# Optimization experiments

Hardware: AMD Instinct MI355X
Metric: run time of the kernel (lower is better)

The kernel has to match this reference:

```python
import jax, jax.numpy as jnp
import numpy as np

B, N, C, D, UP, KNN, MULT, PH = 4, 2048, 256, 64, 4, 20, 4, 64
EPS = 1e-5


def conv1d(x, w, b):
    # x: (B, Cin, N), w: (Cout, Cin)
    return jnp.einsum('oc,bcn->bon', w, x) + b[None, :, None]


def conv2d(x, w, b):
    # x: (B, Cin, N, K), 1x1 conv
    return jnp.einsum('oc,bcnk->bonk', w, x) + b[None, :, None, None]


def bn2d(x, g, bt, rm, rv):
    # eval-mode BatchNorm2d with running stats
    inv = jax.lax.rsqrt(rv + EPS)
    return g[None, :, None, None] * (x - rm[None, :, None, None]) * inv[None, :, None, None] + bt[None, :, None, None]


def group(f, idx):
    # f: (B, C, N), idx: (B, N, K) -> (B, C, N, K)
    return jax.vmap(lambda fb, ib: fb[:, ib])(f, idx)


def setup_inputs() -> dict:
    k0 = jax.random.key(0)
    ks = iter(jax.random.split(k0, 48))
    nx = lambda: next(ks)
    rn = lambda shape, s=0.05: jax.random.normal(nx(), shape, dtype=jnp.float32) * s
    z = lambda n: jnp.zeros((n,), jnp.float32)
    o = lambda n: jnp.ones((n,), jnp.float32)
    inp = {
        'pos': jax.random.normal(nx(), (B, 3, N), dtype=jnp.float32),
        'key': jax.random.normal(nx(), (B, C, N), dtype=jnp.float32),
        'query': jax.random.normal(nx(), (B, C, N), dtype=jnp.float32),
        # MLP_Res (mlp_v): in_dim=2C, hidden=C, out=C
        'wv1': rn((C, 2 * C)), 'bv1': z(C),
        'wv2': rn((C, C)), 'bv2': z(C),
        'wvs': rn((C, 2 * C)), 'bvs': z(C),
        # key/query/value projections to dim D
        'wk': rn((D, C)), 'bk': z(D),
        'wq': rn((D, C)), 'bq': z(D),
        'wval': rn((D, C)), 'bval': z(D),
        # pos_mlp: Conv2d(3,PH) -> BN -> ReLU -> Conv2d(PH,D)
        'pw1': rn((PH, 3)), 'pb1': z(PH), 'pg': o(PH), 'pbt': z(PH), 'prm': z(PH), 'prv': o(PH),
        'pw2': rn((D, PH)), 'pb2': z(D),
        # attn_mlp: Conv2d(D, D*MULT) -> BN -> ReLU -> ConvTranspose2d(D*MULT, D, (UP,1), (UP,1))
        'aw1': rn((D * MULT, D)), 'ab1': z(D * MULT), 'ag': o(D * MULT), 'abt': z(D * MULT), 'arm': z(D * MULT), 'arv': o(D * MULT),
        'ctw': rn((D * MULT, D, UP)), 'ctb': z(D),
        # conv_end: Conv1d(D, C)
        'we': rn((C, D)), 'be': z(C),
    }
    return inp


def reference(pos, key, query, wv1, bv1, wv2, bv2, wvs, bvs, wk, bk, wq, bq, wval, bval,
              pw1, pb1, pg, pbt, prm, prv, pw2, pb2,
              aw1, ab1, ag, abt, arm, arv, ctw, ctb, we, be):
    # mlp_v (MLP_Res) on concat([key, query])
    x = jnp.concatenate([key, query], axis=1)  # (B, 2C, N)
    value = conv1d(jax.nn.relu(conv1d(x, wv1, bv1)), wv2, bv2) + conv1d(x, wvs, bvs)  # (B, C, N)
    identity = value

    k_f = conv1d(key, wk, bk)      # (B, D, N)
    q_f = conv1d(query, wq, bq)    # (B, D, N)
    v_f = conv1d(value, wval, bval)

    # KNN (include_self=True): smallest-KNN indices of pairwise sq distance
    p = jnp.transpose(pos, (0, 2, 1))  # (B, N, 3)
    sq = jnp.sum(p * p, axis=-1)
    dist = sq[:, :, None] + sq[:, None, :] - 2.0 * jnp.einsum('bnc,bmc->bnm', p, p)
    idx = jax.lax.top_k(-dist, KNN)[1]  # (B, N, KNN)

    k_g = group(k_f, idx)                              # (B, D, N, KNN)
    qk_rel = q_f[:, :, :, None] - k_g
    pos_rel = pos[:, :, :, None] - group(pos, idx)     # (B, 3, N, KNN)

    h = jax.nn.relu(bn2d(conv2d(pos_rel, pw1, pb1), pg, pbt, prm, prv))
    pos_emb = conv2d(h, pw2, pb2)                      # (B, D, N, KNN)

    a = jax.nn.relu(bn2d(conv2d(qk_rel + pos_emb, aw1, ab1), ag, abt, arm, arv))  # (B, D*MULT, N, KNN)
    # ConvTranspose2d with kernel=(UP,1), stride=(UP,1): non-overlapping, out[b,o,n*UP+r,k]
    ct = jnp.einsum('bcnk,cor->bornk', a, ctw)         # (B, D, UP, N, KNN)
    Bv = a.shape[0]
    ct = jnp.transpose(ct, (0, 1, 3, 2, 4)).reshape(Bv, D, N * UP, KNN) + ctb[None, :, None, None]
    attn = jax.nn.softmax(ct, axis=-1)                 # softmax over neighbors

    v_g = group(v_f, idx) + pos_emb                    # (B, D, N, KNN)
    v_up = jnp.repeat(v_g, UP, axis=2)                 # nearest Upsample (UP,1)
    agg = jnp.sum(attn * v_up, axis=-1)                # (B, D, N*UP)
    y = conv1d(agg, we, be)                            # (B, C, N*UP)
    return y + jnp.repeat(identity, UP, axis=2)
```

## Files before the change

kernel.cpp:

```cpp
#include <hip/hip_runtime.h>
#include <hip/hip_bf16.h>

#define Bq 4
#define Nq 2048
#define Cq 256
#define Dq 64
#define UPq 4
#define KNNq 20
#define PHq 64
#define DMq 256
#define PTS 16

typedef __attribute__((ext_vector_type(8))) short short8;
typedef __attribute__((ext_vector_type(4))) short short4v;
typedef __attribute__((ext_vector_type(4))) float f32x4;
typedef __hip_bfloat16 bf16;

__device__ __forceinline__ void ld16(float* d, const float* s){
  *reinterpret_cast<float4*>(d) = *reinterpret_cast<const float4*>(s);
}
__device__ __forceinline__ unsigned short f2b(float x){
  bf16 h = __float2bfloat16(x);
  return *reinterpret_cast<unsigned short*>(&h);
}
__device__ __forceinline__ float b2f(short s){
  return __bfloat162float(*reinterpret_cast<bf16*>(&s));
}

__device__ __forceinline__ void swz(const float* __restrict__ src,
                                    short* __restrict__ dst,
                                    int M, int K, int g, bool transp)
{
  int j = g & 7, lane = (g >> 3) & 63, rest = g >> 9;
  int KS = K >> 5;
  int ks = rest % KS, mt = rest / KS;
  int m = mt*16 + (lane & 15);
  int k = ks*32 + ((lane >> 4) << 3) + j;
  float v = transp ? src[k*M + m] : src[m*K + k];
  dst[g] = (short)f2b(v);
}

__global__ __launch_bounds__(256) void k_prep(
    const float* __restrict__ aw1, const float* __restrict__ ctw,
    const float* __restrict__ wv1, const float* __restrict__ wvs,
    const float* __restrict__ wv2, const float* __restrict__ wk,
    const float* __restrict__ wq,  const float* __restrict__ wval,
    const float* __restrict__ pw2, const float* __restrict__ we,
    short* __restrict__ aw1b, short* __restrict__ ctwT,
    short* __restrict__ wv1b, short* __restrict__ wvsb,
    short* __restrict__ wv2b, short* __restrict__ wkb,
    short* __restrict__ wqb,  short* __restrict__ wvalb,
    short* __restrict__ pw2b, short* __restrict__ web)
{
  const int t = threadIdx.x, bidx = blockIdx.x;
  if (bidx < 512){
    swz(wv1, wv1b, 256, 512, bidx*256 + t, false);
  } else if (bidx < 1024){
    swz(wvs, wvsb, 256, 512, (bidx-512)*256 + t, false);
  } else if (bidx < 1280){
    swz(wv2, wv2b, 256, 256, (bidx-1024)*256 + t, false);
  } else if (bidx < 1344){
    swz(wk, wkb, 64, 256, (bidx-1280)*256 + t, false);
  } else if (bidx < 1408){
    swz(wq, wqb, 64, 256, (bidx-1344)*256 + t, false);
  } else if (bidx < 1472){
    swz(wval, wvalb, 64, 256, (bidx-1408)*256 + t, false);
  } else if (bidx < 1488){
    swz(pw2, pw2b, 64, 64, (bidx-1472)*256 + t, false);
  } else if (bidx < 1552){
    swz(aw1, aw1b, 256, 64, (bidx-1488)*256 + t, false);
  } else if (bidx < 1616){
    swz(we, web, 256, 64, (bidx-1552)*256 + t, false);
  } else {
    swz(ctw, ctwT, 256, 256, (bidx-1616)*256 + t, true);
  }
}

__global__ __launch_bounds__(256) void k_value(
    const float* __restrict__ key, const float* __restrict__ query,
    const short* __restrict__ wv1b, const short* __restrict__ wvsb,
    const short* __restrict__ wv2b, const short* __restrict__ wkb,
    const short* __restrict__ wqb,  const short* __restrict__ wvalb,
    const float* __restrict__ bv1, const float* __restrict__ bv2,
    const float* __restrict__ bvs, const float* __restrict__ bk,
    const float* __restrict__ bq,  const float* __restrict__ bval,
    float* __restrict__ valueT, short* __restrict__ kfT,
    short* __restrict__ qfT,    short* __restrict__ vfT)
{
  __shared__ __align__(16) short Xb[16*520];
  __shared__ __align__(16) short hidB[16*264];
  __shared__ __align__(16) short valB[16*264];
  __shared__ __align__(16) float valF[16*264];
  const int t = threadIdx.x;
  const int b = blockIdx.x >> 7;
  const int n0 = (blockIdx.x & 127) * PTS;
  const int lane = t & 63, quad = lane >> 4, l15 = lane & 15, w = t >> 6;

  {
    const int c4 = t >> 2, pq = t & 3;
    #pragma unroll
    for (int pass=0; pass<4; pass++){
      int c = pass*64 + c4;
      float4 kv = *reinterpret_cast<const float4*>(key   + ((size_t)(b*Cq+c))*Nq + n0 + pq*4);
      float4 qv = *reinterpret_cast<const float4*>(query + ((size_t)(b*Cq+c))*Nq + n0 + pq*4);
      const float* kf_ = (const float*)&kv;
      const float* qf_ = (const float*)&qv;
      #pragma unroll
      for (int i=0;i<4;i++){
        Xb[(pq*4+i)*520 + c]       = (short)f2b(kf_[i]);
        Xb[(pq*4+i)*520 + 256 + c] = (short)f2b(qf_[i]);
      }
    }
  }
  __syncthreads();

  f32x4 acc1[4], accS[4];
  #pragma unroll
  for (int jm=0;jm<4;jm++){ acc1[jm]=(f32x4)0.f; accS[jm]=(f32x4)0.f; }

  #pragma unroll
  for (int ks=0;ks<16;ks++){
    const int kcol = ks*32 + quad*8;
    short8 xb = *reinterpret_cast<const short8*>(&Xb[l15*520 + kcol]);
    #pragma unroll
    for (int jm=0;jm<4;jm++){
      int mt = w*4 + jm;
      short8 a1 = *reinterpret_cast<const short8*>(wv1b + ((mt*16+ks)*64 + lane)*8);
      short8 as = *reinterpret_cast<const short8*>(wvsb + ((mt*16+ks)*64 + lane)*8);
      acc1[jm] = __builtin_amdgcn_mfma_f32_16x16x32_bf16(a1, xb, acc1[jm], 0,0,0);
      accS[jm] = __builtin_amdgcn_mfma_f32_16x16x32_bf16(as, xb, accS[jm], 0,0,0);
    }
  }
  #pragma unroll
  for (int jm=0;jm<4;jm++){
    #pragma unroll
    for (int r=0;r<4;r++){
      int h = (w*4+jm)*16 + quad*4 + r;
      hidB[l15*264 + h] = (short)f2b(fmaxf(acc1[jm][r] + bv1[h], 0.f));
    }
  }
  __syncthreads();

  #pragma unroll
  for (int ks=0;ks<8;ks++){
    const int kcol = ks*32 + quad*8;
    short8 hb = *reinterpret_cast<const short8*>(&hidB[l15*264 + kcol]);
    #pragma unroll
    for (int jm=0;jm<4;jm++){
      int mt = w*4 + jm;
      short8 a = *reinterpret_cast<const short8*>(wv2b + ((mt*8+ks)*64 + lane)*8);
      accS[jm] = __builtin_amdgcn_mfma_f32_16x16x32_bf16(a, hb, accS[jm], 0,0,0);
    }
  }
  #pragma unroll
  for (int jm=0;jm<4;jm++){
    #pragma unroll
    for (int r=0;r<4;r++){
      int c = (w*4+jm)*16 + quad*4 + r;
      float v = accS[jm][r] + bv2[c] + bvs[c];
      valF[l15*264 + c] = v;
      valB[l15*264 + c] = (short)f2b(v);
    }
  }
  __syncthreads();

  #pragma unroll
  for (int p=0;p<PTS;p++)
    valueT[((size_t)(b*Nq + n0 + p))*Cq + t] = valF[p*264 + t];

  {
    f32x4 pk4=(f32x4)0.f, pq4=(f32x4)0.f, pv4=(f32x4)0.f;
    #pragma unroll
    for (int ks=0;ks<8;ks++){
      const int kcol = ks*32 + quad*8;
      short8 xk = *reinterpret_cast<const short8*>(&Xb[l15*520 + kcol]);
      short8 xq = *reinterpret_cast<const short8*>(&Xb[l15*520 + 256 + kcol]);
      short8 xv = *reinterpret_cast<const short8*>(&valB[l15*264 + kcol]);
      short8 ak = *reinterpret_cast<const short8*>(wkb  + ((w*8+ks)*64 + lane)*8);
      short8 aq = *reinterpret_cast<const short8*>(wqb  + ((w*8+ks)*64 + lane)*8);
      short8 av = *reinterpret_cast<const short8*>(wvalb+ ((w*8+ks)*64 + lane)*8);
      pk4 = __builtin_amdgcn_mfma_f32_16x16x32_bf16(ak, xk, pk4, 0,0,0);
      pq4 = __builtin_amdgcn_mfma_f32_16x16x32_bf16(aq, xq, pq4, 0,0,0);
      pv4 = __builtin_amdgcn_mfma_f32_16x16x32_bf16(av, xv, pv4, 0,0,0);
    }
    short4v ok, oq, ov;
    #pragma unroll
    for (int r=0;r<4;r++){
      int o = w*16 + quad*4 + r;
      ok[r] = (short)f2b(pk4[r] + bk[o]);
      oq[r] = (short)f2b(pq4[r] + bq[o]);
      ov[r] = (short)f2b(pv4[r] + bval[o]);
    }
    int n = n0 + l15;
    size_t base = ((size_t)(b*Nq+n))*Dq + w*16 + quad*4;
    *reinterpret_cast<short4v*>(kfT + base) = ok;
    *reinterpret_cast<short4v*>(qfT + base) = oq;
    *reinterpret_cast<short4v*>(vfT + base) = ov;
  }
}

__global__ __launch_bounds__(256) void k_knn(const float* __restrict__ pos,
                                             int* __restrict__ idxT)
{
  const int t = threadIdx.x;
  const int lane = t & 63;
  const int w = t >> 6;
  const int pid = blockIdx.x*4 + w;
  const int b = pid >> 11;
  const int n = pid & (Nq-1);
  const float* px = pos + (size_t)(b*3+0)*Nq;
  const float* py = pos + (size_t)(b*3+1)*Nq;
  const float* pz = pos + (size_t)(b*3+2)*Nq;
  const float xn=px[n], yn=py[n], zn=pz[n];
  const float sqn = __fadd_rn(__fadd_rn(__fmul_rn(xn,xn),__fmul_rn(yn,yn)),__fmul_rn(zn,zn));

  double kd[32];
  #pragma unroll
  for (int i=0;i<32;i++){
    int j = i*64 + lane;
    float x=px[j], y=py[j], z=pz[j];
    float sqj = __fadd_rn(__fadd_rn(__fmul_rn(x,x),__fmul_rn(y,y)),__fmul_rn(z,z));
    float dot = __fadd_rn(__fadd_rn(__fmul_rn(xn,x),__fmul_rn(yn,y)),__fmul_rn(zn,z));
    float d   = __fsub_rn(__fadd_rn(sqn,sqj), __fmul_rn(2.0f,dot));
    unsigned u = __float_as_uint(d);
    u ^= ((unsigned)((int)u >> 31)) | 0x80000000u;
    kd[i] = (double)u * 2048.0 + (double)j;
  }

  const double BIG = 9.0e15;
  double last = -1.0;
  for (int s=0;s<KNNq;s++){
    double c[16];
    #pragma unroll
    for (int i=0;i<16;i++){
      double a0 = (kd[i]    > last) ? kd[i]    : BIG;
      double a1 = (kd[i+16] > last) ? kd[i+16] : BIG;
      c[i] = fmin(a0, a1);
    }
    #pragma unroll
    for (int off=8; off>0; off>>=1){
      #pragma unroll
      for (int i=0;i<off;i++) c[i] = fmin(c[i], c[i+off]);
    }
    double m = c[0];
    #pragma unroll
    for (int off=1; off<64; off<<=1)
      m = fmin(m, __shfl_xor(m, off));
    if (lane == 0){
      unsigned long long kk = (unsigned long long)m;
      idxT[(size_t)pid*KNNq + s] = (int)(kk & 2047ull);
    }
    last = m;
  }
}

__global__ __launch_bounds__(256) void k_attn(
  const float* __restrict__ pos,
  const float* __restrict__ valueT, const short* __restrict__ kfT,
  const short* __restrict__ qfT,    const short* __restrict__ vfT,
  const int* __restrict__ idxT,
  const float* __restrict__ pw1, const float* __restrict__ pb1,
  const float* __restrict__ pg,  const float* __restrict__ pbt,
  const float* __restrict__ prm, const float* __restrict__ prv,
  const short* __restrict__ pw2b, const float* __restrict__ pb2,
  const short* __restrict__ aw1b, const float* __restrict__ ab1,
  const float* __restrict__ ag,  const float* __restrict__ abt,
  const float* __restrict__ arm, const float* __restrict__ arv,
  const short* __restrict__ ctwT,
  const short* __restrict__ web,  const float* __restrict__ be,
  float* __restrict__ out)
{
  __shared__ __align__(16) char  unionA[26624];
  __shared__ __align__(16) char  unionB[6912];
  __shared__ __align__(16) short uT[48*72];
  __shared__ __align__(16) short vgB[64*56];
  __shared__ float scS[DMq], sh2S[DMq];
  __shared__ float prl[3*48];
  __shared__ int   nb[48];

  short* sT   = (short*)unionA;
  short* ctS  = (short*)unionA;
  short* hB   = (short*)unionB;
  short* aggB = (short*)unionB;

  const int t = threadIdx.x;
  const int b  = blockIdx.x >> 10;
  const int n0 = (blockIdx.x & 1023) * 2;
  const int lane = t & 63, quad = lane >> 4, l15 = lane & 15, w = t >> 6;
  const size_t bN = (size_t)b * Nq;

  if (t < 48){
    int p = (t >= 24);
    int k = t - p*24;
    int nn = n0 + p;
    int j = (k < KNNq) ? idxT[(bN + nn)*KNNq + k] : nn;
    nb[t] = j;
    #pragma unroll
    for (int d=0; d<3; d++){
      prl[d*48+t] = pos[((size_t)(b*3+d))*Nq + nn] - pos[((size_t)(b*3+d))*Nq + j];
    }
  }
  {
    float sc = ag[t] * rsqrtf(arv[t] + 1e-5f);
    scS[t]  = sc;
    sh2S[t] = ab1[t]*sc + (abt[t] - arm[t]*sc);
  }
  __syncthreads();

  {
    const int ph = t & 63, pkq = t >> 6;
    float sc = pg[ph] * rsqrtf(prv[ph] + 1e-5f);
    float sh = pbt[ph] - prm[ph] * sc;
    float w0 = pw1[ph*3+0], w1 = pw1[ph*3+1], w2 = pw1[ph*3+2];
    float bb = pb1[ph];
    #pragma unroll
    for (int m=0;m<12;m++){
      int pk = pkq + m*4;
      float h = w0*prl[pk] + w1*prl[48+pk] + w2*prl[96+pk] + bb;
      hB[pk*72 + ph] = (short)f2b(fmaxf(h*sc + sh, 0.f));
    }
  }
  __syncthreads();

  {
    f32x4 accP[3];
    #pragma unroll
    for (int nt=0;nt<3;nt++) accP[nt]=(f32x4)0.f;
    #pragma unroll
    for (int ks=0;ks<2;ks++){
      const int kcol = ks*32 + quad*8;
      short8 a = *reinterpret_cast<const short8*>(pw2b + ((w*2+ks)*64 + lane)*8);
      #pragma unroll
      for (int nt=0;nt<3;nt++){
        short8 bb = *reinterpret_cast<const short8*>(&hB[(nt*16+l15)*72 + kcol]);
        accP[nt] = __builtin_amdgcn_mfma_f32_16x16x32_bf16(a, bb, accP[nt], 0,0,0);
      }
    }
    const int obase = w*16 + quad*4;
    #pragma unroll
    for (int nt=0;nt<3;nt++){
      int pk = nt*16 + l15;
      int p = (pk >= 24);
      int j = nb[pk];
      int nn = n0 + p;
      short4v q4 = *reinterpret_cast<const short4v*>(qfT + (bN+nn)*Dq + obase);
      short4v k4 = *reinterpret_cast<const short4v*>(kfT + (bN+j)*Dq + obase);
      short4v v4 = *reinterpret_cast<const short4v*>(vfT + (bN+j)*Dq + obase);
      #pragma unroll
      for (int r=0;r<4;r++){
        int o = obase + r;
        float pe = accP[nt][r] + pb2[o];
        uT[pk*72 + o]  = (short)f2b((b2f(q4[r]) - b2f(k4[r])) + pe);
        vgB[o*56 + pk] = (short)f2b(b2f(v4[r]) + pe);
      }
    }
  }
  __syncthreads();

  {
    for (int i = t; i < 576; i += 256) aggB[576 + i] = 0;

    f32x4 accC[4][3];
    #pragma unroll
    for (int jm=0;jm<4;jm++)
      #pragma unroll
      for (int nt=0;nt<3;nt++) accC[jm][nt]=(f32x4)0.f;
    #pragma unroll
    for (int ks=0;ks<2;ks++){
      const int kcol = ks*32 + quad*8;
      short8 bb[3];
      #pragma unroll
      for (int nt=0;nt<3;nt++)
        bb[nt] = *reinterpret_cast<const short8*>(&uT[(nt*16+l15)*72 + kcol]);
      #pragma unroll
      for (int jm=0;jm<4;jm++){
        int mt = w*4 + jm;
        short8 a = *reinterpret_cast<const short8*>(aw1b + ((mt*2+ks)*64 + lane)*8);
        #pragma unroll
        for (int nt=0;nt<3;nt++)
          accC[jm][nt] = __builtin_amdgcn_mfma_f32_16x16x32_bf16(a, bb[nt], accC[jm][nt], 0,0,0);
      }
    }
    #pragma unroll
    for (int jm=0;jm<4;jm++){
      int cb = (w*4+jm)*16 + quad*4;
      #pragma unroll
      for (int nt=0;nt<3;nt++){
        int pk = nt*16 + l15;
        short4v pkv;
        #pragma unroll
        for (int r=0;r<4;r++){
          int c = cb + r;
          pkv[r] = (short)f2b(fmaxf(accC[jm][nt][r]*scS[c] + sh2S[c], 0.f));
        }
        *reinterpret_cast<short4v*>(&sT[pk*264 + cb]) = pkv;
      }
    }
  }
  __syncthreads();

  {
    f32x4 accT[4][3];
    #pragma unroll
    for (int jm=0;jm<4;jm++)
      #pragma unroll
      for (int nt=0;nt<3;nt++) accT[jm][nt]=(f32x4)0.f;
    #pragma unroll
    for (int ks=0;ks<8;ks++){
      const int kcol = ks*32 + quad*8;
      short8 bb[3];
      #pragma unroll
      for (int nt=0;nt<3;nt++)
        bb[nt] = *reinterpret_cast<const short8*>(&sT[(nt*16+l15)*264 + kcol]);
      #pragma unroll
      for (int jm=0;jm<4;jm++){
        int mt = w*4 + jm;
        short8 a = *reinterpret_cast<const short8*>(ctwT + ((mt*8+ks)*64 + lane)*8);
        #pragma unroll
        for (int nt=0;nt<3;nt++)
          accT[jm][nt] = __builtin_amdgcn_mfma_f32_16x16x32_bf16(a, bb[nt], accT[jm][nt], 0,0,0);
      }
    }
    __syncthreads();
    #pragma unroll
    for (int jm=0;jm<4;jm++){
      #pragma unroll
      for (int nt=0;nt<3;nt++){
        int pk = nt*16 + l15;
        #pragma unroll
        for (int r=0;r<4;r++){
          int row = (w*4+jm)*16 + quad*4 + r;
          ctS[row*52 + pk] = (short)f2b(accT[jm][nt][r]);
        }
      }
    }
  }
  __syncthreads();

  {
    int o = t >> 2, rr = t & 3;
    #pragma unroll
    for (int p=0;p<2;p++){
      float ct[20], vgv[20];
      #pragma unroll
      for (int q=0;q<5;q++){
        short4v cv  = *reinterpret_cast<const short4v*>(&ctS[t*52 + p*24 + q*4]);
        short4v vv4 = *reinterpret_cast<const short4v*>(&vgB[o*56 + p*24 + q*4]);
        #pragma unroll
        for (int i=0;i<4;i++){ ct[q*4+i]=b2f(cv[i]); vgv[q*4+i]=b2f(vv4[i]); }
      }
      float m = ct[0];
      #pragma unroll
      for (int k=1;k<20;k++) m = fmaxf(m, ct[k]);
      float s = 0.f, a = 0.f;
      #pragma unroll
      for (int k=0;k<20;k++){
        float e = __expf(ct[k]-m);
        s += e;
        a = fmaf(e, vgv[k], a);
      }
      aggB[(p*4+rr)*72 + o] = (short)f2b(a/s);
    }
  }
  __syncthreads();

  {
    f32x4 accE[4];
    #pragma unroll
    for (int jm=0;jm<4;jm++) accE[jm]=(f32x4)0.f;
    #pragma unroll
    for (int ks=0;ks<2;ks++){
      const int kcol = ks*32 + quad*8;
      short8 bb = *reinterpret_cast<const short8*>(&aggB[l15*72 + kcol]);
      #pragma unroll
      for (int jm=0;jm<4;jm++){
        int mt = w*4 + jm;
        short8 a = *reinterpret_cast<const short8*>(web + ((mt*2+ks)*64 + lane)*8);
        accE[jm] = __builtin_amdgcn_mfma_f32_16x16x32_bf16(a, bb, accE[jm], 0,0,0);
      }
    }
    if (l15 < 8){
      int p = l15 >> 2, rr = l15 & 3;
      #pragma unroll
      for (int jm=0;jm<4;jm++){
        #pragma unroll
        for (int r=0;r<4;r++){
          int c = (w*4+jm)*16 + quad*4 + r;
          float y = accE[jm][r] + be[c] + valueT[(bN + n0 + p)*Cq + c];
          out[((size_t)(b*Cq+c))*((size_t)Nq*UPq) + (size_t)(n0+p)*UPq + rr] = y;
        }
      }
    }
  }
}

extern "C" void kernel_launch(void* const* d_in, const int* in_sizes, int n_in,
                              void* d_out, int out_size, void* d_ws, size_t ws_size,
                              hipStream_t stream)
{
  const float* pos  = (const float*)d_in[0];
  const float* key  = (const float*)d_in[1];
  const float* qry  = (const float*)d_in[2];
  const float* wv1  = (const float*)d_in[3];
  const float* bv1  = (const float*)d_in[4];
  const float* wv2  = (const float*)d_in[5];
  const float* bv2  = (const float*)d_in[6];
  const float* wvs  = (const float*)d_in[7];
  const float* bvs  = (const float*)d_in[8];
  const float* wk   = (const float*)d_in[9];
  const float* bk   = (const float*)d_in[10];
  const float* wq   = (const float*)d_in[11];
  const float* bq   = (const float*)d_in[12];
  const float* wval = (const float*)d_in[13];
  const float* bval = (const float*)d_in[14];
  const float* pw1  = (const float*)d_in[15];
  const float* pb1  = (const float*)d_in[16];
  const float* pg   = (const float*)d_in[17];
  const float* pbt  = (const float*)d_in[18];
  const float* prm  = (const float*)d_in[19];
  const float* prv  = (const float*)d_in[20];
  const float* pw2  = (const float*)d_in[21];
  const float* pb2  = (const float*)d_in[22];
  const float* aw1  = (const float*)d_in[23];
  const float* ab1  = (const float*)d_in[24];
  const float* ag   = (const float*)d_in[25];
  const float* abt  = (const float*)d_in[26];
  const float* arm  = (const float*)d_in[27];
  const float* arv  = (const float*)d_in[28];
  const float* ctw  = (const float*)d_in[29];
  const float* we   = (const float*)d_in[31];
  const float* be   = (const float*)d_in[32];

  char* ws = (char*)d_ws;
  float* valueT = (float*)(ws);
  short* kfT    = (short*)(ws + 8388608);
  short* qfT    = (short*)(ws + 9437184);
  short* vfT    = (short*)(ws + 10485760);
  int*   idxT   = (int*)  (ws + 11534336);
  short* aw1b   = (short*)(ws + 12189696);
  short* ctwT   = (short*)(ws + 12222464);
  short* wv1b   = (short*)(ws + 12353536);
  short* wvsb   = (short*)(ws + 12615680);
  short* wv2b   = (short*)(ws + 12877824);
  short* wkb    = (short*)(ws + 13008896);
  short* wqb    = (short*)(ws + 13041664);
  short* wvalb  = (short*)(ws + 13074432);
  short* pw2b   = (short*)(ws + 13107200);
  short* web    = (short*)(ws + 13115392);
  float* out    = (float*)d_out;

  k_prep<<<dim3(1872), dim3(256), 0, stream>>>(
      aw1, ctw, wv1, wvs, wv2, wk, wq, wval, pw2, we,
      aw1b, ctwT, wv1b, wvsb, wv2b, wkb, wqb, wvalb, pw2b, web);
  k_value<<<dim3(Bq*Nq/PTS), dim3(256), 0, stream>>>(
      key, qry, wv1b, wvsb, wv2b, wkb, wqb, wvalb,
      bv1, bv2, bvs, bk, bq, bval,
      valueT, kfT, qfT, vfT);
  k_knn<<<dim3(Bq*Nq/4), dim3(256), 0, stream>>>(pos, idxT);
  k_attn<<<dim3(Bq*Nq/2), dim3(256), 0, stream>>>(
      pos, valueT, kfT, qfT, vfT, idxT,
      pw1, pb1, pg, pbt, prm, prv, pw2b, pb2,
      aw1b, ab1, ag, abt, arm, arv, ctwT, web, be, out);
}
```

Measured before the change: 286.5 us.

## Shrink attention kernel LDS footprint via chunked MLP, swizzling, and BN folding

Restructures k_attn so the attn_mlp hidden activations are produced and consumed in two 128-channel chunks, which lets the shared-memory buffers shrink and be unioned, and sets launch bounds to target 4 blocks per CU. LDS layouts switch from padded strides to XOR-swizzled addressing. BatchNorm scale is folded into aw1 during prep and into pw1 inside the kernel. Neighbor gathers and identity loads are issued early to hide latency, and only the 20 valid neighbor columns are stored. The trade-off is an extra barrier per chunk and higher register pressure from the hoisted loads.

```diff
diff --git a/kernel.cpp b/kernel.cpp
--- a/kernel.cpp
+++ b/kernel.cpp
@@ -40,6 +40,21 @@
   dst[g] = (short)f2b(v);
 }
 
+__device__ __forceinline__ void swz_s(const float* __restrict__ src,
+                                      short* __restrict__ dst,
+                                      int M, int K, int g,
+                                      const float* __restrict__ gam,
+                                      const float* __restrict__ var)
+{
+  int j = g & 7, lane = (g >> 3) & 63, rest = g >> 9;
+  int KS = K >> 5;
+  int ks = rest % KS, mt = rest / KS;
+  int m = mt*16 + (lane & 15);
+  int k = ks*32 + ((lane >> 4) << 3) + j;
+  float sc = gam[m] * rsqrtf(var[m] + 1e-5f);
+  dst[g] = (short)f2b(src[m*K + k] * sc);
+}
+
 __global__ __launch_bounds__(256) void k_prep(
     const float* __restrict__ aw1, const float* __restrict__ ctw,
     const float* __restrict__ wv1, const float* __restrict__ wvs,
@@ -50,7 +65,8 @@
     short* __restrict__ wv1b, short* __restrict__ wvsb,
     short* __restrict__ wv2b, short* __restrict__ wkb,
     short* __restrict__ wqb,  short* __restrict__ wvalb,
-    short* __restrict__ pw2b, short* __restrict__ web)
+    short* __restrict__ pw2b, short* __restrict__ web,
+    const float* __restrict__ ag, const float* __restrict__ arv)
 {
   const int t = threadIdx.x, bidx = blockIdx.x;
   if (bidx < 512){
@@ -68,7 +84,7 @@
   } else if (bidx < 1488){
     swz(pw2, pw2b, 64, 64, (bidx-1472)*256 + t, false);
   } else if (bidx < 1552){
-    swz(aw1, aw1b, 256, 64, (bidx-1488)*256 + t, false);
+    swz_s(aw1, aw1b, 256, 64, (bidx-1488)*256 + t, ag, arv);
   } else if (bidx < 1616){
     swz(we, web, 256, 64, (bidx-1552)*256 + t, false);
   } else {
@@ -254,7 +270,10 @@
   }
 }
 
-__global__ __launch_bounds__(256) void k_attn(
+#define UADDR(row, colb) ((((row)*128 + (colb)) ^ (((row)&7)<<4)))
+#define SADDR(row, colb) ((((row)*256 + (colb)) ^ (((row)&7)<<4)))
+
+__global__ __launch_bounds__(256, 4) void k_attn(
   const float* __restrict__ pos,
   const float* __restrict__ valueT, const short* __restrict__ kfT,
   const short* __restrict__ qfT,    const short* __restrict__ vfT,
@@ -270,24 +289,21 @@
   const short* __restrict__ web,  const float* __restrict__ be,
   float* __restrict__ out)
 {
-  __shared__ __align__(16) char  unionA[26624];
-  __shared__ __align__(16) char  unionB[6912];
-  __shared__ __align__(16) short uT[48*72];
-  __shared__ __align__(16) short vgB[64*56];
-  __shared__ float scS[DMq], sh2S[DMq];
-  __shared__ float prl[3*48];
-  __shared__ int   nb[48];
-
-  short* sT   = (short*)unionA;
-  short* ctS  = (short*)unionA;
-  short* hB   = (short*)unionB;
-  short* aggB = (short*)unionB;
+  __shared__ __align__(16) char unionA[22528];
+  __shared__ __align__(16) char unionB[6144];
+  __shared__ __align__(16) char unionC[6144];
+  __shared__ __align__(16) short vgB[64*40];
+
+  float* sh2S = (float*)(unionA + 12288);
+  float* prl  = (float*)unionC;
+  int*   nb   = (int*)(unionC + 576);
 
   const int t = threadIdx.x;
   const int b  = blockIdx.x >> 10;
   const int n0 = (blockIdx.x & 1023) * 2;
   const int lane = t & 63, quad = lane >> 4, l15 = lane & 15, w = t >> 6;
   const size_t bN = (size_t)b * Nq;
+  const int obase = w*16 + quad*4;
 
   if (t < 48){
     int p = (t >= 24);
@@ -302,22 +318,31 @@
   }
   {
     float sc = ag[t] * rsqrtf(arv[t] + 1e-5f);
-    scS[t]  = sc;
-    sh2S[t] = ab1[t]*sc + (abt[t] - arm[t]*sc);
-  }
-  __syncthreads();
+    sh2S[t]  = ab1[t]*sc + (abt[t] - arm[t]*sc);
+  }
+  __syncthreads();
+
+  short4v pq4[3], pk4[3], pv4[3];
+  #pragma unroll
+  for (int nt=0; nt<3; nt++){
+    int pk = nt*16 + l15;
+    int p  = (pk >= 24);
+    int j  = nb[pk];
+    pq4[nt] = *reinterpret_cast<const short4v*>(qfT + (bN + n0 + p)*Dq + obase);
+    pk4[nt] = *reinterpret_cast<const short4v*>(kfT + (bN + j)*Dq + obase);
+    pv4[nt] = *reinterpret_cast<const short4v*>(vfT + (bN + j)*Dq + obase);
+  }
 
   {
-    const int ph = t & 63, pkq = t >> 6;
+    const int ph = t & 63;
     float sc = pg[ph] * rsqrtf(prv[ph] + 1e-5f);
-    float sh = pbt[ph] - prm[ph] * sc;
-    float w0 = pw1[ph*3+0], w1 = pw1[ph*3+1], w2 = pw1[ph*3+2];
-    float bb = pb1[ph];
+    float w0 = pw1[ph*3+0]*sc, w1 = pw1[ph*3+1]*sc, w2 = pw1[ph*3+2]*sc;
+    float bb = pb1[ph]*sc + (pbt[ph] - prm[ph]*sc);
     #pragma unroll
     for (int m=0;m<12;m++){
-      int pk = pkq + m*4;
-      float h = w0*prl[pk] + w1*prl[48+pk] + w2*prl[96+pk] + bb;
-      hB[pk*72 + ph] = (short)f2b(fmaxf(h*sc + sh, 0.f));
+      int pk = w + m*4;
+      float h = fmaf(w0, prl[pk], fmaf(w1, prl[48+pk], fmaf(w2, prl[96+pk], bb)));
+      *(short*)(unionB + UADDR(pk, ph*2)) = (short)f2b(fmaxf(h, 0.f));
     }
   }
   __syncthreads();
@@ -328,138 +353,148 @@
     for (int nt=0;nt<3;nt++) accP[nt]=(f32x4)0.f;
     #pragma unroll
     for (int ks=0;ks<2;ks++){
-      const int kcol = ks*32 + quad*8;
+      const int kcolb = (ks*32 + quad*8)*2;
       short8 a = *reinterpret_cast<const short8*>(pw2b + ((w*2+ks)*64 + lane)*8);
       #pragma unroll
       for (int nt=0;nt<3;nt++){
-        short8 bb = *reinterpret_cast<const short8*>(&hB[(nt*16+l15)*72 + kcol]);
+        short8 bb = *reinterpret_cast<const short8*>(unionB + UADDR(nt*16+l15, kcolb));
         accP[nt] = __builtin_amdgcn_mfma_f32_16x16x32_bf16(a, bb, accP[nt], 0,0,0);
       }
     }
-    const int obase = w*16 + quad*4;
     #pragma unroll
     for (int nt=0;nt<3;nt++){
       int pk = nt*16 + l15;
-      int p = (pk >= 24);
-      int j = nb[pk];
-      int nn = n0 + p;
-      short4v q4 = *reinterpret_cast<const short4v*>(qfT + (bN+nn)*Dq + obase);
-      short4v k4 = *reinterpret_cast<const short4v*>(kfT + (bN+j)*Dq + obase);
-      short4v v4 = *reinterpret_cast<const short4v*>(vfT + (bN+j)*Dq + obase);
+      bool vld = (pk < 20) || (pk >= 24 && pk < 44);
+      int col  = pk - (pk >= 24 ? 4 : 0);
+      short4v ut4;
       #pragma unroll
       for (int r=0;r<4;r++){
         int o = obase + r;
         float pe = accP[nt][r] + pb2[o];
-        uT[pk*72 + o]  = (short)f2b((b2f(q4[r]) - b2f(k4[r])) + pe);
-        vgB[o*56 + pk] = (short)f2b(b2f(v4[r]) + pe);
-      }
-    }
-  }
-  __syncthreads();
-
-  {
-    for (int i = t; i < 576; i += 256) aggB[576 + i] = 0;
-
-    f32x4 accC[4][3];
-    #pragma unroll
-    for (int jm=0;jm<4;jm++)
+        ut4[r] = (short)f2b((b2f(pq4[nt][r]) - b2f(pk4[nt][r])) + pe);
+        if (vld) vgB[o*40 + col] = (short)f2b(b2f(pv4[nt][r]) + pe);
+      }
+      *(short4v*)(unionC + UADDR(pk, obase*2)) = ut4;
+    }
+  }
+  __syncthreads();
+
+  f32x4 accT[4][3];
+  #pragma unroll
+  for (int jm=0;jm<4;jm++)
+    #pragma unroll
+    for (int nt=0;nt<3;nt++) accT[jm][nt]=(f32x4)0.f;
+
+  #pragma unroll
+  for (int ch=0; ch<2; ch++){
+    f32x4 accC[2][3];
+    #pragma unroll
+    for (int jm=0;jm<2;jm++)
       #pragma unroll
       for (int nt=0;nt<3;nt++) accC[jm][nt]=(f32x4)0.f;
     #pragma unroll
     for (int ks=0;ks<2;ks++){
-      const int kcol = ks*32 + quad*8;
+      const int kcolb = (ks*32 + quad*8)*2;
       short8 bb[3];
       #pragma unroll
       for (int nt=0;nt<3;nt++)
-        bb[nt] = *reinterpret_cast<const short8*>(&uT[(nt*16+l15)*72 + kcol]);
-      #pragma unroll
-      for (int jm=0;jm<4;jm++){
-        int mt = w*4 + jm;
+        bb[nt] = *reinterpret_cast<const short8*>(unionC + UADDR(nt*16+l15, kcolb));
+      #pragma unroll
+      for (int jm=0;jm<2;jm++){
+        int mt = ch*8 + w*2 + jm;
         short8 a = *reinterpret_cast<const short8*>(aw1b + ((mt*2+ks)*64 + lane)*8);
         #pragma unroll
         for (int nt=0;nt<3;nt++)
           accC[jm][nt] = __builtin_amdgcn_mfma_f32_16x16x32_bf16(a, bb[nt], accC[jm][nt], 0,0,0);
       }
     }
-    #pragma unroll
-    for (int jm=0;jm<4;jm++){
-      int cb = (w*4+jm)*16 + quad*4;
+    if (ch == 1) __syncthreads();
+    #pragma unroll
+    for (int jm=0;jm<2;jm++){
+      const int colb = ((w*2+jm)*16 + quad*4)*2;
       #pragma unroll
       for (int nt=0;nt<3;nt++){
         int pk = nt*16 + l15;
         short4v pkv;
         #pragma unroll
         for (int r=0;r<4;r++){
-          int c = cb + r;
-          pkv[r] = (short)f2b(fmaxf(accC[jm][nt][r]*scS[c] + sh2S[c], 0.f));
+          int c = ch*128 + (w*2+jm)*16 + quad*4 + r;
+          pkv[r] = (short)f2b(fmaxf(accC[jm][nt][r] + sh2S[c], 0.f));
         }
-        *reinterpret_cast<short4v*>(&sT[pk*264 + cb]) = pkv;
-      }
-    }
-  }
-  __syncthreads();
-
-  {
-    f32x4 accT[4][3];
-    #pragma unroll
-    for (int jm=0;jm<4;jm++)
-      #pragma unroll
-      for (int nt=0;nt<3;nt++) accT[jm][nt]=(f32x4)0.f;
-    #pragma unroll
-    for (int ks=0;ks<8;ks++){
-      const int kcol = ks*32 + quad*8;
+        *(short4v*)(unionA + SADDR(pk, colb)) = pkv;
+      }
+    }
+    __syncthreads();
+    #pragma unroll
+    for (int ksl=0; ksl<4; ksl++){
+      const int kcolb = (ksl*32 + quad*8)*2;
       short8 bb[3];
       #pragma unroll
       for (int nt=0;nt<3;nt++)
-        bb[nt] = *reinterpret_cast<const short8*>(&sT[(nt*16+l15)*264 + kcol]);
+        bb[nt] = *reinterpret_cast<const short8*>(unionA + SADDR(nt*16+l15, kcolb));
       #pragma unroll
       for (int jm=0;jm<4;jm++){
         int mt = w*4 + jm;
-        short8 a = *reinterpret_cast<const short8*>(ctwT + ((mt*8+ks)*64 + lane)*8);
+        short8 a = *reinterpret_cast<const short8*>(ctwT + ((mt*8 + ch*4 + ksl)*64 + lane)*8);
         #pragma unroll
         for (int nt=0;nt<3;nt++)
           accT[jm][nt] = __builtin_amdgcn_mfma_f32_16x16x32_bf16(a, bb[nt], accT[jm][nt], 0,0,0);
       }
     }
-    __syncthreads();
-    #pragma unroll
-    for (int jm=0;jm<4;jm++){
-      #pragma unroll
-      for (int nt=0;nt<3;nt++){
-        int pk = nt*16 + l15;
+  }
+  __syncthreads();
+
+  #pragma unroll
+  for (int nt=0;nt<3;nt++){
+    int pk = nt*16 + l15;
+    bool vld = (pk < 20) || (pk >= 24 && pk < 44);
+    int col  = pk - (pk >= 24 ? 4 : 0);
+    if (vld){
+      #pragma unroll
+      for (int jm=0;jm<4;jm++){
         #pragma unroll
         for (int r=0;r<4;r++){
           int row = (w*4+jm)*16 + quad*4 + r;
-          ctS[row*52 + pk] = (short)f2b(accT[jm][nt][r]);
+          *(short*)(unionA + row*88 + col*2) = (short)f2b(accT[jm][nt][r]);
         }
       }
     }
   }
   __syncthreads();
 
+  float4 idv[4];
+  if (l15 < 8){
+    int p = l15 >> 2;
+    #pragma unroll
+    for (int jm=0;jm<4;jm++)
+      idv[jm] = *reinterpret_cast<const float4*>(valueT + (bN + n0 + p)*Cq + (w*4+jm)*16 + quad*4);
+  }
   {
-    int o = t >> 2, rr = t & 3;
+    const int o = t >> 2, rr = t & 3;
     #pragma unroll
     for (int p=0;p<2;p++){
-      float ct[20], vgv[20];
+      float ct[20];
       #pragma unroll
       for (int q=0;q<5;q++){
-        short4v cv  = *reinterpret_cast<const short4v*>(&ctS[t*52 + p*24 + q*4]);
-        short4v vv4 = *reinterpret_cast<const short4v*>(&vgB[o*56 + p*24 + q*4]);
+        short4v cv = *reinterpret_cast<const short4v*>(unionA + t*88 + p*40 + q*8);
         #pragma unroll
-        for (int i=0;i<4;i++){ ct[q*4+i]=b2f(cv[i]); vgv[q*4+i]=b2f(vv4[i]); }
+        for (int i=0;i<4;i++) ct[q*4+i] = b2f(cv[i]);
       }
       float m = ct[0];
       #pragma unroll
       for (int k=1;k<20;k++) m = fmaxf(m, ct[k]);
       float s = 0.f, a = 0.f;
       #pragma unroll
-      for (int k=0;k<20;k++){
-        float e = __expf(ct[k]-m);
-        s += e;
-        a = fmaf(e, vgv[k], a);
-      }
-      aggB[(p*4+rr)*72 + o] = (short)f2b(a/s);
+      for (int q=0;q<5;q++){
+        short4v vv = *reinterpret_cast<const short4v*>((const char*)vgB + o*80 + p*40 + q*8);
+        #pragma unroll
+        for (int i=0;i<4;i++){
+          float e = __expf(ct[q*4+i] - m);
+          s += e;
+          a = fmaf(e, b2f(vv[i]), a);
+        }
+      }
+      *(short*)(unionB + UADDR(p*4+rr, o*2)) = (short)f2b(__fdividef(a, s));
     }
   }
   __syncthreads();
@@ -470,8 +505,8 @@
     for (int jm=0;jm<4;jm++) accE[jm]=(f32x4)0.f;
     #pragma unroll
     for (int ks=0;ks<2;ks++){
-      const int kcol = ks*32 + quad*8;
-      short8 bb = *reinterpret_cast<const short8*>(&aggB[l15*72 + kcol]);
+      const int kcolb = (ks*32 + quad*8)*2;
+      short8 bb = *reinterpret_cast<const short8*>(unionB + UADDR(l15, kcolb));
       #pragma unroll
       for (int jm=0;jm<4;jm++){
         int mt = w*4 + jm;
@@ -483,10 +518,11 @@
       int p = l15 >> 2, rr = l15 & 3;
       #pragma unroll
       for (int jm=0;jm<4;jm++){
+        float4 b4 = *reinterpret_cast<const float4*>(be + (w*4+jm)*16 + quad*4);
         #pragma unroll
         for (int r=0;r<4;r++){
           int c = (w*4+jm)*16 + quad*4 + r;
-          float y = accE[jm][r] + be[c] + valueT[(bN + n0 + p)*Cq + c];
+          float y = accE[jm][r] + ((const float*)&b4)[r] + ((const float*)&idv[jm])[r];
           out[((size_t)(b*Cq+c))*((size_t)Nq*UPq) + (size_t)(n0+p)*UPq + rr] = y;
         }
       }
@@ -551,7 +587,8 @@
 
   k_prep<<<dim3(1872), dim3(256), 0, stream>>>(
       aw1, ctw, wv1, wvs, wv2, wk, wq, wval, pw2, we,
-      aw1b, ctwT, wv1b, wvsb, wv2b, wkb, wqb, wvalb, pw2b, web);
+      aw1b, ctwT, wv1b, wvsb, wv2b, wkb, wqb, wvalb, pw2b, web,
+      ag, arv);
   k_value<<<dim3(Bq*Nq/PTS), dim3(256), 0, stream>>>(
       key, qry, wv1b, wvsb, wv2b, wkb, wqb, wvalb,
       bv1, bv2, bvs, bk, bq, bval,
```

Measured after the change: 285.3 us. Within noise of the previous version (-0.4%).
